# Optimization experiments

Hardware: AMD Instinct MI355X
Metric: run time of the kernel (lower is better)

The kernel has to match this reference:

```python
import jax, jax.numpy as jnp
import numpy as np

EMBED = 1024
HEADS = 16
HEAD = EMBED // HEADS
B, S = 8, 1024


def setup_inputs() -> dict:
    key = jax.random.key(0)
    ks = jax.random.split(key, 12)
    inp = {
        "values": jax.random.normal(ks[0], (B, S, EMBED), jnp.float32),
        "keys": jax.random.normal(ks[1], (B, S, EMBED), jnp.float32),
        "query": jax.random.normal(ks[2], (B, S, EMBED), jnp.float32),
        # causal mask broadcastable to [B, heads, q, k]
        "mask": jnp.broadcast_to(jnp.tril(jnp.ones((S, S), jnp.int32))[None, None], (B, 1, S, S)),
        "Wv": jax.random.normal(ks[3], (HEAD, HEAD), jnp.float32) / np.sqrt(HEAD),
        "bv": jnp.zeros((HEAD,), jnp.float32),
        "Wk": jax.random.normal(ks[4], (HEAD, HEAD), jnp.float32) / np.sqrt(HEAD),
        "bk": jnp.zeros((HEAD,), jnp.float32),
        "Wq": jax.random.normal(ks[5], (HEAD, HEAD), jnp.float32) / np.sqrt(HEAD),
        "bq": jnp.zeros((HEAD,), jnp.float32),
        "Wfc": jax.random.normal(ks[6], (EMBED, EMBED), jnp.float32) / np.sqrt(EMBED),
        "bfc": jnp.zeros((EMBED,), jnp.float32),
    }
    return inp


def reference(values, keys, query, mask, Wv, bv, Wk, bk, Wq, bq, Wfc, bfc):
    N, q_len = query.shape[0], query.shape[1]
    k_len, v_len = keys.shape[1], values.shape[1]
    # split heads: [N, S, H, D]
    v = values.reshape(N, v_len, HEADS, HEAD)
    k = keys.reshape(N, k_len, HEADS, HEAD)
    q = query.reshape(N, q_len, HEADS, HEAD)
    # per-head linear projections (torch Linear: x @ W.T + b)
    v = v @ Wv.T + bv
    k = k @ Wk.T + bk
    q = q @ Wq.T + bq
    # scores [N, H, q, k]
    scores = jnp.einsum('nqhz,nkhz->nhqk', q, k)
    scores = jnp.where(mask == 0, -jnp.inf, scores)
    # NOTE: original divides by sqrt(query_size) (sequence length), not head dim
    attn = jax.nn.softmax(scores / jnp.sqrt(jnp.float32(q_len)), axis=-1)
    out = jnp.einsum('nhqk,nkhz->nqhz', attn, v).reshape(N, q_len, HEADS * HEAD)
    return out @ Wfc.T + bfc
```

## Files before the change

kernel.cpp:

```cpp
#include <hip/hip_runtime.h>
#include <stdint.h>

typedef __attribute__((ext_vector_type(8))) short short8;
typedef __attribute__((ext_vector_type(4))) short short4v;
typedef __attribute__((ext_vector_type(4))) float floatx4;
typedef __attribute__((ext_vector_type(4))) unsigned short ushort4v;

#define HEADS 16
#define HEAD 64
#define SEQ 1024
#define BATCH 8

__device__ __forceinline__ unsigned short f2bf(float f) {
    union { float f; unsigned int u; } v; v.f = f;
    unsigned int r = v.u + 0x7FFFu + ((v.u >> 16) & 1u);
    return (unsigned short)(r >> 16);
}

__device__ __forceinline__ void gload_lds16(const void* g, void* l) {
    __builtin_amdgcn_global_load_lds((const __attribute__((address_space(1))) void*)g,
                                     (__attribute__((address_space(3))) void*)l, 16, 0, 0);
}

__global__ __launch_bounds__(256) void cvt_kernel(const float* __restrict__ in,
                                                  unsigned short* __restrict__ out) {
    int i = (blockIdx.x * 256 + threadIdx.x) * 4;
    float4 f = *(const float4*)(in + i);
    ushort4v v;
    v.x = f2bf(f.x); v.y = f2bf(f.y); v.z = f2bf(f.z); v.w = f2bf(f.w);
    *(ushort4v*)(out + i) = v;
}

__global__ __launch_bounds__(256) void proj_kernel(
    const float* __restrict__ Vin, const float* __restrict__ Kin, const float* __restrict__ Qin,
    const float* __restrict__ Wv, const float* __restrict__ bv,
    const float* __restrict__ Wk, const float* __restrict__ bk,
    const float* __restrict__ Wq, const float* __restrict__ bq,
    unsigned short* __restrict__ q_ws, unsigned short* __restrict__ k_ws,
    unsigned short* __restrict__ v_ws)
{
    const int tid = threadIdx.x;
    const int tile = blockIdx.x;
    const int ph = blockIdx.y;
    const int proj = ph >> 4;
    const int h = ph & 15;

    const float* X; const float* W; const float* bias;
    if (proj == 0)      { X = Qin; W = Wq; bias = bq; }
    else if (proj == 1) { X = Kin; W = Wk; bias = bk; }
    else                { X = Vin; W = Wv; bias = bv; }

    __shared__ unsigned short sX[64 * 64];
    __shared__ unsigned short sW[64 * 64];

    const int m0 = tile * 64;
    {
        int r = tid >> 2, c = (tid & 3) * 16;
        const float4* xs = (const float4*)(X + (size_t)(m0 + r) * 1024 + h * 64 + c);
        const float4* wsrc = (const float4*)(W + r * 64 + c);
        unsigned short* dX = sX + r * 64 + c;
        unsigned short* dW = sW + r * 64 + c;
#pragma unroll
        for (int i = 0; i < 4; ++i) {
            float4 fx = xs[i];
            float4 fw = wsrc[i];
            dX[i*4+0] = f2bf(fx.x); dX[i*4+1] = f2bf(fx.y); dX[i*4+2] = f2bf(fx.z); dX[i*4+3] = f2bf(fx.w);
            dW[i*4+0] = f2bf(fw.x); dW[i*4+1] = f2bf(fw.y); dW[i*4+2] = f2bf(fw.z); dW[i*4+3] = f2bf(fw.w);
        }
    }
    __syncthreads();

    const int wave = tid >> 6, lane = tid & 63;
    const int lq = lane & 15, quad = lane >> 4;

    const floatx4 zero4 = {0.f, 0.f, 0.f, 0.f};
    floatx4 acc[4] = {zero4, zero4, zero4, zero4};

    short8 afr[2];
    afr[0] = *(const short8*)(sX + (wave * 16 + lq) * 64 + quad * 8);
    afr[1] = *(const short8*)(sX + (wave * 16 + lq) * 64 + quad * 8 + 32);
#pragma unroll
    for (int ks = 0; ks < 2; ++ks) {
#pragma unroll
        for (int nt = 0; nt < 4; ++nt) {
            short8 bfr = *(const short8*)(sW + (nt * 16 + lq) * 64 + quad * 8 + ks * 32);
            acc[nt] = __builtin_amdgcn_mfma_f32_16x16x32_bf16(afr[ks], bfr, acc[nt], 0, 0, 0);
        }
    }
    __syncthreads();
#pragma unroll
    for (int nt = 0; nt < 4; ++nt) {
        int d = nt * 16 + lq;
        float bcol = bias[d];
#pragma unroll
        for (int r = 0; r < 4; ++r) {
            int srow = wave * 16 + quad * 4 + r;
            sX[srow * 64 + d] = f2bf(acc[nt][r] + bcol);
        }
    }
    __syncthreads();

    const int b = m0 >> 10, s0 = m0 & 1023;
    if (proj < 2) {
        unsigned short* dstb = (proj == 0 ? q_ws : k_ws);
        int r = tid >> 2, c = (tid & 3) * 16;
        unsigned short* dst = dstb + ((size_t)((b * 16 + h) * 1024 + s0 + r)) * 64 + c;
        const short4v* src = (const short4v*)(sX + r * 64 + c);
        ((short4v*)dst)[0] = src[0];
        ((short4v*)dst)[1] = src[1];
        ((short4v*)dst)[2] = src[2];
        ((short4v*)dst)[3] = src[3];
    } else {
        int d = tid >> 2, c = (tid & 3) * 16;
        short8 v0, v1;
#pragma unroll
        for (int j = 0; j < 8; ++j) v0[j] = (short)sX[(c + j) * 64 + d];
#pragma unroll
        for (int j = 0; j < 8; ++j) v1[j] = (short)sX[(c + 8 + j) * 64 + d];
        unsigned short* dst = v_ws + ((size_t)((b * 16 + h) * 64 + d)) * 1024 + s0 + c;
        ((short8*)dst)[0] = v0;
        ((short8*)dst)[1] = v1;
    }
}

__global__ __launch_bounds__(256) void attn_kernel(
    const unsigned short* __restrict__ q_ws, const unsigned short* __restrict__ k_ws,
    const unsigned short* __restrict__ v_ws, unsigned short* __restrict__ attn_ws)
{
    const int bh = blockIdx.x;
    const int qt = blockIdx.y;
    const int b = bh >> 4, h = bh & 15;
    const int tid = threadIdx.x;
    const int wave = tid >> 6, lane = tid & 63;
    const int lq = lane & 15, quad = lane >> 4;

    __shared__ unsigned short sK[64 * 64];
    __shared__ unsigned short sV[64 * 64];
    __shared__ unsigned short sP[4][16 * 64];

    const size_t head_off = (size_t)bh * SEQ * HEAD;
    const unsigned short* qb = q_ws + head_off;
    const unsigned short* kb = k_ws + head_off;
    const unsigned short* vb = v_ws + head_off;

    short8 aq[2];
    {
        int qrow = qt * 64 + wave * 16 + lq;
        const unsigned short* qp = qb + (size_t)qrow * 64 + quad * 8;
        aq[0] = *(const short8*)(qp);
        aq[1] = *(const short8*)(qp + 32);
    }

    const floatx4 zero4 = {0.f, 0.f, 0.f, 0.f};
    floatx4 o[4] = {zero4, zero4, zero4, zero4};
    float m_i[4], l_i[4];
#pragma unroll
    for (int i = 0; i < 4; ++i) { m_i[i] = -__builtin_inff(); l_i[i] = 0.f; }

    const float scale = 0.03125f * 1.44269504088896340736f;

    for (int kt = 0; kt <= qt; ++kt) {
        {
            const char* kt_base = (const char*)(kb + (size_t)kt * 64 * 64);
#pragma unroll
            for (int issue = 0; issue < 2; ++issue) {
                int off = (issue * 4 + wave) * 1024 + lane * 16;
                gload_lds16(kt_base + off, (char*)sK + (issue * 4 + wave) * 1024);
            }
#pragma unroll
            for (int issue = 0; issue < 2; ++issue) {
                int off = (issue * 4 + wave) * 1024 + lane * 16;
                int drow = off >> 7;
                int sbyte = off & 127;
                const char* g = (const char*)vb + (size_t)drow * 2048 + (size_t)kt * 128 + sbyte;
                gload_lds16(g, (char*)sV + (issue * 4 + wave) * 1024);
            }
        }
        __syncthreads();

        floatx4 sfr[4] = {zero4, zero4, zero4, zero4};
#pragma unroll
        for (int ks = 0; ks < 2; ++ks) {
#pragma unroll
            for (int nt = 0; nt < 4; ++nt) {
                short8 bfr = *(const short8*)(sK + (nt * 16 + lq) * 64 + quad * 8 + ks * 32);
                sfr[nt] = __builtin_amdgcn_mfma_f32_16x16x32_bf16(aq[ks], bfr, sfr[nt], 0, 0, 0);
            }
        }

        float t[4][4];
#pragma unroll
        for (int nt = 0; nt < 4; ++nt) {
#pragma unroll
            for (int r = 0; r < 4; ++r) {
                float val = sfr[nt][r] * scale;
                if (kt == qt) {
                    int kg = nt * 16 + lq;
                    int qg = wave * 16 + quad * 4 + r;
                    if (kg > qg) val = -__builtin_inff();
                }
                t[nt][r] = val;
            }
        }

        float alpha[4];
#pragma unroll
        for (int r = 0; r < 4; ++r) {
            float rm = fmaxf(fmaxf(t[0][r], t[1][r]), fmaxf(t[2][r], t[3][r]));
#pragma unroll
            for (int mk = 1; mk < 16; mk <<= 1) rm = fmaxf(rm, __shfl_xor(rm, mk, 64));
            float mnew = fmaxf(m_i[r], rm);
            alpha[r] = exp2f(m_i[r] - mnew);
            m_i[r] = mnew;
            float p0 = exp2f(t[0][r] - mnew);
            float p1 = exp2f(t[1][r] - mnew);
            float p2 = exp2f(t[2][r] - mnew);
            float p3 = exp2f(t[3][r] - mnew);
            t[0][r] = p0; t[1][r] = p1; t[2][r] = p2; t[3][r] = p3;
            float s = p0 + p1 + p2 + p3;
#pragma unroll
            for (int mk = 1; mk < 16; mk <<= 1) s += __shfl_xor(s, mk, 64);
            l_i[r] = l_i[r] * alpha[r] + s;
        }

#pragma unroll
        for (int nt = 0; nt < 4; ++nt) {
#pragma unroll
            for (int r = 0; r < 4; ++r) {
                sP[wave][(quad * 4 + r) * 64 + nt * 16 + lq] = f2bf(t[nt][r]);
            }
        }
#pragma unroll
        for (int nt = 0; nt < 4; ++nt) {
#pragma unroll
            for (int r = 0; r < 4; ++r) o[nt][r] *= alpha[r];
        }
        asm volatile("s_waitcnt lgkmcnt(0)" ::: "memory");

#pragma unroll
        for (int ks = 0; ks < 2; ++ks) {
            short8 pa = *(const short8*)(&sP[wave][lq * 64 + quad * 8 + ks * 32]);
#pragma unroll
            for (int nt = 0; nt < 4; ++nt) {
                short8 bfr = *(const short8*)(sV + (nt * 16 + lq) * 64 + quad * 8 + ks * 32);
                o[nt] = __builtin_amdgcn_mfma_f32_16x16x32_bf16(pa, bfr, o[nt], 0, 0, 0);
            }
        }
        __syncthreads();
    }

#pragma unroll
    for (int r = 0; r < 4; ++r) l_i[r] = 1.f / l_i[r];
    const int srow_base = qt * 64 + wave * 16 + quad * 4;
#pragma unroll
    for (int nt = 0; nt < 4; ++nt) {
        int col = h * 64 + nt * 16 + lq;
#pragma unroll
        for (int r = 0; r < 4; ++r) {
            int srow = srow_base + r;
            attn_ws[((size_t)(b * SEQ + srow)) * 1024 + col] = f2bf(o[nt][r] * l_i[r]);
        }
    }
}

__global__ __launch_bounds__(256) void fc_kernel(
    const unsigned short* __restrict__ A, const unsigned short* __restrict__ Bw,
    const float* __restrict__ bias, float* __restrict__ out)
{
    const int nt0 = blockIdx.x * 128;
    const int mt0 = blockIdx.y * 128;
    const int tid = threadIdx.x;
    const int wave = tid >> 6, lane = tid & 63;
    const int lq = lane & 15, quad = lane >> 4;
    const int wm = (wave >> 1) * 64, wn = (wave & 1) * 64;

    __shared__ unsigned short sA[128 * 32];
    __shared__ unsigned short sB[128 * 32];

    const floatx4 zero4 = {0.f, 0.f, 0.f, 0.f};
    floatx4 acc[4][4];
#pragma unroll
    for (int i = 0; i < 4; ++i)
#pragma unroll
        for (int j = 0; j < 4; ++j) acc[i][j] = zero4;

    for (int kt = 0; kt < 32; ++kt) {
#pragma unroll
        for (int issue = 0; issue < 2; ++issue) {
            int off = (issue * 4 + wave) * 1024 + lane * 16;
            int row = off >> 6;
            int cb = off & 63;
            const char* ga = (const char*)A + (size_t)(mt0 + row) * 2048 + kt * 64 + cb;
            gload_lds16(ga, (char*)sA + (issue * 4 + wave) * 1024);
            const char* gb = (const char*)Bw + (size_t)(nt0 + row) * 2048 + kt * 64 + cb;
            gload_lds16(gb, (char*)sB + (issue * 4 + wave) * 1024);
        }
        __syncthreads();

        short8 af[4], bf[4];
#pragma unroll
        for (int i = 0; i < 4; ++i) {
            af[i] = *(const short8*)(sA + (wm + i * 16 + lq) * 32 + quad * 8);
            bf[i] = *(const short8*)(sB + (wn + i * 16 + lq) * 32 + quad * 8);
        }
#pragma unroll
        for (int mi = 0; mi < 4; ++mi)
#pragma unroll
            for (int ni = 0; ni < 4; ++ni)
                acc[mi][ni] = __builtin_amdgcn_mfma_f32_16x16x32_bf16(af[mi], bf[ni], acc[mi][ni], 0, 0, 0);
        __syncthreads();
    }

#pragma unroll
    for (int mi = 0; mi < 4; ++mi) {
#pragma unroll
        for (int ni = 0; ni < 4; ++ni) {
            int col = nt0 + wn + ni * 16 + lq;
            float bc = bias[col];
#pragma unroll
            for (int r = 0; r < 4; ++r) {
                int row = mt0 + wm + mi * 16 + quad * 4 + r;
                out[(size_t)row * 1024 + col] = acc[mi][ni][r] + bc;
            }
        }
    }
}

extern "C" void kernel_launch(void* const* d_in, const int* in_sizes, int n_in,
                              void* d_out, int out_size, void* d_ws, size_t ws_size,
                              hipStream_t stream)
{
    const float* values = (const float*)d_in[0];
    const float* keys   = (const float*)d_in[1];
    const float* query  = (const float*)d_in[2];
    const float* Wv  = (const float*)d_in[4];
    const float* bv  = (const float*)d_in[5];
    const float* Wk  = (const float*)d_in[6];
    const float* bk  = (const float*)d_in[7];
    const float* Wq  = (const float*)d_in[8];
    const float* bq  = (const float*)d_in[9];
    const float* Wfc = (const float*)d_in[10];
    const float* bfc = (const float*)d_in[11];
    float* out = (float*)d_out;

    char* ws = (char*)d_ws;
    unsigned short* q_ws    = (unsigned short*)(ws);
    unsigned short* k_ws    = (unsigned short*)(ws + (16u << 20));
    unsigned short* v_ws    = (unsigned short*)(ws + (32u << 20));
    unsigned short* attn_ws = (unsigned short*)(ws + (48u << 20));
    unsigned short* wfc_ws  = (unsigned short*)(ws + (64u << 20));

    cvt_kernel<<<dim3(1024), dim3(256), 0, stream>>>(Wfc, wfc_ws);
    proj_kernel<<<dim3(128, 48), dim3(256), 0, stream>>>(
        values, keys, query, Wv, bv, Wk, bk, Wq, bq, q_ws, k_ws, v_ws);
    attn_kernel<<<dim3(128, 16), dim3(256), 0, stream>>>(q_ws, k_ws, v_ws, attn_ws);
    fc_kernel<<<dim3(8, 64), dim3(256), 0, stream>>>(attn_ws, wfc_ws, bfc, out);
}
```

Measured before the change: 299.5 us.

## Drop online max, balance causal tiles, read K/V from global in attention

The attention kernel now handles two query tiles per block (qt and 15-qt) to balance causal work, and launches half as many blocks. It drops the running-max rescaling and shuffle reductions in favour of exponentiating scaled scores directly. Row sums are computed with an MFMA against a ones vector. K and V fragments are read straight from global memory instead of staged through LDS, and the P buffer is XOR-swizzled. The projection kernel builds A fragments in registers, swizzles the weight tile in LDS and pads the output tile. Skipping max subtraction risks overflow for large scores, and the direct global K/V loads repeat per-wave traffic that LDS staging used to share.

```diff
diff --git a/kernel.cpp b/kernel.cpp
--- a/kernel.cpp
+++ b/kernel.cpp
@@ -50,44 +50,59 @@
     else if (proj == 1) { X = Kin; W = Wk; bias = bk; }
     else                { X = Vin; W = Wv; bias = bv; }
 
-    __shared__ unsigned short sX[64 * 64];
     __shared__ unsigned short sW[64 * 64];
-
-    const int m0 = tile * 64;
-    {
-        int r = tid >> 2, c = (tid & 3) * 16;
-        const float4* xs = (const float4*)(X + (size_t)(m0 + r) * 1024 + h * 64 + c);
-        const float4* wsrc = (const float4*)(W + r * 64 + c);
-        unsigned short* dX = sX + r * 64 + c;
-        unsigned short* dW = sW + r * 64 + c;
-#pragma unroll
-        for (int i = 0; i < 4; ++i) {
-            float4 fx = xs[i];
-            float4 fw = wsrc[i];
-            dX[i*4+0] = f2bf(fx.x); dX[i*4+1] = f2bf(fx.y); dX[i*4+2] = f2bf(fx.z); dX[i*4+3] = f2bf(fx.w);
-            dW[i*4+0] = f2bf(fw.x); dW[i*4+1] = f2bf(fw.y); dW[i*4+2] = f2bf(fw.z); dW[i*4+3] = f2bf(fw.w);
-        }
-    }
-    __syncthreads();
+    __shared__ unsigned short sX[64 * 72];
 
     const int wave = tid >> 6, lane = tid & 63;
     const int lq = lane & 15, quad = lane >> 4;
+    const int m0 = tile * 64;
+
+    {
+        int n = tid >> 2, c0 = (tid & 3) * 16;
+        const float* wr = W + n * 64 + c0;
+#pragma unroll
+        for (int half = 0; half < 2; ++half) {
+            float4 fa = *(const float4*)(wr + half * 8);
+            float4 fb = *(const float4*)(wr + half * 8 + 4);
+            short8 v;
+            v[0] = (short)f2bf(fa.x); v[1] = (short)f2bf(fa.y);
+            v[2] = (short)f2bf(fa.z); v[3] = (short)f2bf(fa.w);
+            v[4] = (short)f2bf(fb.x); v[5] = (short)f2bf(fb.y);
+            v[6] = (short)f2bf(fb.z); v[7] = (short)f2bf(fb.w);
+            int chunk = ((c0 >> 3) + half) ^ (n & 7);
+            *(short8*)&sW[n * 64 + chunk * 8] = v;
+        }
+    }
+
+    short8 afr[2];
+    {
+        const float* xr = X + (size_t)(m0 + wave * 16 + lq) * 1024 + h * 64;
+#pragma unroll
+        for (int ks = 0; ks < 2; ++ks) {
+            float4 f0 = *(const float4*)(xr + quad * 8 + ks * 32);
+            float4 f1 = *(const float4*)(xr + quad * 8 + ks * 32 + 4);
+            short8 a;
+            a[0] = (short)f2bf(f0.x); a[1] = (short)f2bf(f0.y);
+            a[2] = (short)f2bf(f0.z); a[3] = (short)f2bf(f0.w);
+            a[4] = (short)f2bf(f1.x); a[5] = (short)f2bf(f1.y);
+            a[6] = (short)f2bf(f1.z); a[7] = (short)f2bf(f1.w);
+            afr[ks] = a;
+        }
+    }
+    __syncthreads();
 
     const floatx4 zero4 = {0.f, 0.f, 0.f, 0.f};
     floatx4 acc[4] = {zero4, zero4, zero4, zero4};
-
-    short8 afr[2];
-    afr[0] = *(const short8*)(sX + (wave * 16 + lq) * 64 + quad * 8);
-    afr[1] = *(const short8*)(sX + (wave * 16 + lq) * 64 + quad * 8 + 32);
 #pragma unroll
     for (int ks = 0; ks < 2; ++ks) {
 #pragma unroll
         for (int nt = 0; nt < 4; ++nt) {
-            short8 bfr = *(const short8*)(sW + (nt * 16 + lq) * 64 + quad * 8 + ks * 32);
+            int n = nt * 16 + lq;
+            short8 bfr = *(const short8*)&sW[n * 64 + (((quad + 4 * ks) ^ (n & 7)) * 8)];
             acc[nt] = __builtin_amdgcn_mfma_f32_16x16x32_bf16(afr[ks], bfr, acc[nt], 0, 0, 0);
         }
     }
-    __syncthreads();
+
 #pragma unroll
     for (int nt = 0; nt < 4; ++nt) {
         int d = nt * 16 + lq;
@@ -95,7 +110,7 @@
 #pragma unroll
         for (int r = 0; r < 4; ++r) {
             int srow = wave * 16 + quad * 4 + r;
-            sX[srow * 64 + d] = f2bf(acc[nt][r] + bcol);
+            sX[srow * 72 + d] = f2bf(acc[nt][r] + bcol);
         }
     }
     __syncthreads();
@@ -105,160 +120,119 @@
         unsigned short* dstb = (proj == 0 ? q_ws : k_ws);
         int r = tid >> 2, c = (tid & 3) * 16;
         unsigned short* dst = dstb + ((size_t)((b * 16 + h) * 1024 + s0 + r)) * 64 + c;
-        const short4v* src = (const short4v*)(sX + r * 64 + c);
-        ((short4v*)dst)[0] = src[0];
-        ((short4v*)dst)[1] = src[1];
-        ((short4v*)dst)[2] = src[2];
-        ((short4v*)dst)[3] = src[3];
+        const unsigned short* src = sX + r * 72 + c;
+        ((short4v*)dst)[0] = *(const short4v*)(src);
+        ((short4v*)dst)[1] = *(const short4v*)(src + 4);
+        ((short4v*)dst)[2] = *(const short4v*)(src + 8);
+        ((short4v*)dst)[3] = *(const short4v*)(src + 12);
     } else {
         int d = tid >> 2, c = (tid & 3) * 16;
         short8 v0, v1;
 #pragma unroll
-        for (int j = 0; j < 8; ++j) v0[j] = (short)sX[(c + j) * 64 + d];
-#pragma unroll
-        for (int j = 0; j < 8; ++j) v1[j] = (short)sX[(c + 8 + j) * 64 + d];
+        for (int j = 0; j < 8; ++j) v0[j] = (short)sX[(c + j) * 72 + d];
+#pragma unroll
+        for (int j = 0; j < 8; ++j) v1[j] = (short)sX[(c + 8 + j) * 72 + d];
         unsigned short* dst = v_ws + ((size_t)((b * 16 + h) * 64 + d)) * 1024 + s0 + c;
-        ((short8*)dst)[0] = v0;
-        ((short8*)dst)[1] = v1;
-    }
-}
-
-__global__ __launch_bounds__(256) void attn_kernel(
+        *(short8*)dst = v0;
+        *(short8*)(dst + 8) = v1;
+    }
+}
+
+__global__ __launch_bounds__(256, 4) void attn_kernel(
     const unsigned short* __restrict__ q_ws, const unsigned short* __restrict__ k_ws,
     const unsigned short* __restrict__ v_ws, unsigned short* __restrict__ attn_ws)
 {
     const int bh = blockIdx.x;
-    const int qt = blockIdx.y;
     const int b = bh >> 4, h = bh & 15;
     const int tid = threadIdx.x;
     const int wave = tid >> 6, lane = tid & 63;
     const int lq = lane & 15, quad = lane >> 4;
 
-    __shared__ unsigned short sK[64 * 64];
-    __shared__ unsigned short sV[64 * 64];
-    __shared__ unsigned short sP[4][16 * 64];
+    __shared__ unsigned short sP[4][1024];
 
     const size_t head_off = (size_t)bh * SEQ * HEAD;
     const unsigned short* qb = q_ws + head_off;
     const unsigned short* kb = k_ws + head_off;
     const unsigned short* vb = v_ws + head_off;
 
-    short8 aq[2];
-    {
-        int qrow = qt * 64 + wave * 16 + lq;
-        const unsigned short* qp = qb + (size_t)qrow * 64 + quad * 8;
-        aq[0] = *(const short8*)(qp);
-        aq[1] = *(const short8*)(qp + 32);
-    }
-
+    short8 ones;
+#pragma unroll
+    for (int j = 0; j < 8; ++j) ones[j] = (short)0x3F80;
+
+    const float scale2 = 0.03125f * 1.44269504088896340736f;
     const floatx4 zero4 = {0.f, 0.f, 0.f, 0.f};
-    floatx4 o[4] = {zero4, zero4, zero4, zero4};
-    float m_i[4], l_i[4];
-#pragma unroll
-    for (int i = 0; i < 4; ++i) { m_i[i] = -__builtin_inff(); l_i[i] = 0.f; }
-
-    const float scale = 0.03125f * 1.44269504088896340736f;
-
-    for (int kt = 0; kt <= qt; ++kt) {
+
+    for (int pass = 0; pass < 2; ++pass) {
+        const int qt = pass ? (15 - blockIdx.y) : blockIdx.y;
+
+        short8 aq[2];
         {
-            const char* kt_base = (const char*)(kb + (size_t)kt * 64 * 64);
-#pragma unroll
-            for (int issue = 0; issue < 2; ++issue) {
-                int off = (issue * 4 + wave) * 1024 + lane * 16;
-                gload_lds16(kt_base + off, (char*)sK + (issue * 4 + wave) * 1024);
-            }
-#pragma unroll
-            for (int issue = 0; issue < 2; ++issue) {
-                int off = (issue * 4 + wave) * 1024 + lane * 16;
-                int drow = off >> 7;
-                int sbyte = off & 127;
-                const char* g = (const char*)vb + (size_t)drow * 2048 + (size_t)kt * 128 + sbyte;
-                gload_lds16(g, (char*)sV + (issue * 4 + wave) * 1024);
-            }
-        }
-        __syncthreads();
-
-        floatx4 sfr[4] = {zero4, zero4, zero4, zero4};
-#pragma unroll
-        for (int ks = 0; ks < 2; ++ks) {
+            const unsigned short* qp = qb + (size_t)(qt * 64 + wave * 16 + lq) * 64 + quad * 8;
+            aq[0] = *(const short8*)qp;
+            aq[1] = *(const short8*)(qp + 32);
+        }
+
+        floatx4 o[4] = {zero4, zero4, zero4, zero4};
+        floatx4 lacc = zero4;
+
+        for (int kt = 0; kt <= qt; ++kt) {
+            const unsigned short* kbase = kb + (size_t)(kt * 64 + lq) * 64 + quad * 8;
+            floatx4 s[4] = {zero4, zero4, zero4, zero4};
+#pragma unroll
+            for (int ks = 0; ks < 2; ++ks) {
+#pragma unroll
+                for (int nt = 0; nt < 4; ++nt) {
+                    short8 kf = *(const short8*)(kbase + nt * 1024 + ks * 32);
+                    s[nt] = __builtin_amdgcn_mfma_f32_16x16x32_bf16(aq[ks], kf, s[nt], 0, 0, 0);
+                }
+            }
+
+            float t[4][4];
 #pragma unroll
             for (int nt = 0; nt < 4; ++nt) {
-                short8 bfr = *(const short8*)(sK + (nt * 16 + lq) * 64 + quad * 8 + ks * 32);
-                sfr[nt] = __builtin_amdgcn_mfma_f32_16x16x32_bf16(aq[ks], bfr, sfr[nt], 0, 0, 0);
-            }
-        }
-
-        float t[4][4];
+#pragma unroll
+                for (int r = 0; r < 4; ++r) {
+                    float p = __builtin_amdgcn_exp2f(s[nt][r] * scale2);
+                    if (kt == qt && (nt * 16 + lq) > (wave * 16 + quad * 4 + r)) p = 0.f;
+                    t[nt][r] = p;
+                }
+            }
+
+            unsigned short* wp = &sP[wave][0];
+#pragma unroll
+            for (int nt = 0; nt < 4; ++nt) {
+                int ch = (((nt * 2 + (lq >> 3)) ^ (quad << 1)) * 8) + (lq & 7);
+#pragma unroll
+                for (int r = 0; r < 4; ++r) {
+                    wp[(quad * 4 + r) * 64 + ch] = f2bf(t[nt][r]);
+                }
+            }
+            asm volatile("s_waitcnt lgkmcnt(0)" ::: "memory");
+
+            const unsigned short* vbase = vb + (size_t)lq * 1024 + kt * 64 + quad * 8;
+#pragma unroll
+            for (int ks = 0; ks < 2; ++ks) {
+                short8 pa = *(const short8*)&sP[wave][lq * 64 + (((quad + 4 * ks) ^ ((lq >> 2) << 1)) * 8)];
+                lacc = __builtin_amdgcn_mfma_f32_16x16x32_bf16(pa, ones, lacc, 0, 0, 0);
+#pragma unroll
+                for (int nt = 0; nt < 4; ++nt) {
+                    short8 vf = *(const short8*)(vbase + nt * 16384 + ks * 32);
+                    o[nt] = __builtin_amdgcn_mfma_f32_16x16x32_bf16(pa, vf, o[nt], 0, 0, 0);
+                }
+            }
+        }
+
+        float inv[4];
+#pragma unroll
+        for (int r = 0; r < 4; ++r) inv[r] = 1.f / lacc[r];
+        const int srow_base = qt * 64 + wave * 16 + quad * 4;
 #pragma unroll
         for (int nt = 0; nt < 4; ++nt) {
+            int col = h * 64 + nt * 16 + lq;
 #pragma unroll
             for (int r = 0; r < 4; ++r) {
-                float val = sfr[nt][r] * scale;
-                if (kt == qt) {
-                    int kg = nt * 16 + lq;
-                    int qg = wave * 16 + quad * 4 + r;
-                    if (kg > qg) val = -__builtin_inff();
-                }
-                t[nt][r] = val;
-            }
-        }
-
-        float alpha[4];
-#pragma unroll
-        for (int r = 0; r < 4; ++r) {
-            float rm = fmaxf(fmaxf(t[0][r], t[1][r]), fmaxf(t[2][r], t[3][r]));
-#pragma unroll
-            for (int mk = 1; mk < 16; mk <<= 1) rm = fmaxf(rm, __shfl_xor(rm, mk, 64));
-            float mnew = fmaxf(m_i[r], rm);
-            alpha[r] = exp2f(m_i[r] - mnew);
-            m_i[r] = mnew;
-            float p0 = exp2f(t[0][r] - mnew);
-            float p1 = exp2f(t[1][r] - mnew);
-            float p2 = exp2f(t[2][r] - mnew);
-            float p3 = exp2f(t[3][r] - mnew);
-            t[0][r] = p0; t[1][r] = p1; t[2][r] = p2; t[3][r] = p3;
-            float s = p0 + p1 + p2 + p3;
-#pragma unroll
-            for (int mk = 1; mk < 16; mk <<= 1) s += __shfl_xor(s, mk, 64);
-            l_i[r] = l_i[r] * alpha[r] + s;
-        }
-
-#pragma unroll
-        for (int nt = 0; nt < 4; ++nt) {
-#pragma unroll
-            for (int r = 0; r < 4; ++r) {
-                sP[wave][(quad * 4 + r) * 64 + nt * 16 + lq] = f2bf(t[nt][r]);
-            }
-        }
-#pragma unroll
-        for (int nt = 0; nt < 4; ++nt) {
-#pragma unroll
-            for (int r = 0; r < 4; ++r) o[nt][r] *= alpha[r];
-        }
-        asm volatile("s_waitcnt lgkmcnt(0)" ::: "memory");
-
-#pragma unroll
-        for (int ks = 0; ks < 2; ++ks) {
-            short8 pa = *(const short8*)(&sP[wave][lq * 64 + quad * 8 + ks * 32]);
-#pragma unroll
-            for (int nt = 0; nt < 4; ++nt) {
-                short8 bfr = *(const short8*)(sV + (nt * 16 + lq) * 64 + quad * 8 + ks * 32);
-                o[nt] = __builtin_amdgcn_mfma_f32_16x16x32_bf16(pa, bfr, o[nt], 0, 0, 0);
-            }
-        }
-        __syncthreads();
-    }
-
-#pragma unroll
-    for (int r = 0; r < 4; ++r) l_i[r] = 1.f / l_i[r];
-    const int srow_base = qt * 64 + wave * 16 + quad * 4;
-#pragma unroll
-    for (int nt = 0; nt < 4; ++nt) {
-        int col = h * 64 + nt * 16 + lq;
-#pragma unroll
-        for (int r = 0; r < 4; ++r) {
-            int srow = srow_base + r;
-            attn_ws[((size_t)(b * SEQ + srow)) * 1024 + col] = f2bf(o[nt][r] * l_i[r]);
+                attn_ws[((size_t)(b * SEQ + srow_base + r)) * 1024 + col] = f2bf(o[nt][r] * inv[r]);
+            }
         }
     }
 }
@@ -353,6 +327,6 @@
     cvt_kernel<<<dim3(1024), dim3(256), 0, stream>>>(Wfc, wfc_ws);
     proj_kernel<<<dim3(128, 48), dim3(256), 0, stream>>>(
         values, keys, query, Wv, bv, Wk, bk, Wq, bq, q_ws, k_ws, v_ws);
-    attn_kernel<<<dim3(128, 16), dim3(256), 0, stream>>>(q_ws, k_ws, v_ws, attn_ws);
+    attn_kernel<<<dim3(128, 8), dim3(256), 0, stream>>>(q_ws, k_ws, v_ws, attn_ws);
     fc_kernel<<<dim3(8, 64), dim3(256), 0, stream>>>(attn_ws, wfc_ws, bfc, out);
 }
```

Result: slower. 333.2 us (+11.3%).
